# Performance work log

Hardware: AMD Instinct MI355X
Metric: run time of the kernel (lower is better)

The kernel has to match this reference:

```python
import jax, jax.numpy as jnp
import numpy as np

K = 3          # number of nearest neighbors (init kwarg k)
EPS = 1e-16    # PyG knn_interpolate clamps squared distance at 1e-16


def setup_inputs() -> dict:
    key = jax.random.key(0)
    ks = jax.random.split(key, 8)
    N, M, C_IN, C_SKIP, H = 4096, 16384, 256, 128, 256
    x = jax.random.normal(ks[0], (N, C_IN), dtype=jnp.float32)
    pos = jax.random.normal(ks[1], (N, 3), dtype=jnp.float32)
    x_skip = jax.random.normal(ks[2], (M, C_SKIP), dtype=jnp.float32)
    pos_skip = jax.random.normal(ks[3], (M, 3), dtype=jnp.float32)
    W1 = jax.random.normal(ks[4], (C_IN + C_SKIP, H), dtype=jnp.float32) * (1.0 / np.sqrt(C_IN + C_SKIP))
    b1 = jnp.zeros((H,), dtype=jnp.float32)
    W2 = jax.random.normal(ks[5], (H, H), dtype=jnp.float32) * (1.0 / np.sqrt(H))
    b2 = jnp.zeros((H,), dtype=jnp.float32)
    return {"x": x, "pos": pos, "x_skip": x_skip, "pos_skip": pos_skip,
            "W1": W1, "b1": b1, "W2": W2, "b2": b2}


def knn_interpolate(x, pos, pos_skip):
    # squared pairwise distances [M, N]
    d2 = (jnp.sum(pos_skip * pos_skip, -1, keepdims=True)
          - 2.0 * pos_skip @ pos.T
          + jnp.sum(pos * pos, -1))
    neg_d, idx = jax.lax.top_k(-d2, K)          # k smallest distances
    w = 1.0 / jnp.maximum(-neg_d, EPS)           # [M, K] inverse-distance weights
    feats = x[idx]                               # [M, K, C] gather
    return jnp.einsum('mk,mkc->mc', w, feats) / jnp.sum(w, -1, keepdims=True)


def reference(x, pos, x_skip, pos_skip, W1, b1, W2, b2):
    y = knn_interpolate(x, pos, pos_skip)                # [M, C_in]
    h = jnp.concatenate([y, x_skip], axis=-1)            # [M, C_in + C_skip]
    h = jax.nn.relu(h @ W1 + b1)
    return h @ W2 + b2                                    # [M, H]
```

## Files before the change

kernel.cpp:

```cpp
#include <hip/hip_runtime.h>
#include <hip/hip_bf16.h>

#define N_PTS 4096
#define M_PTS 16384
#define CIN   256
#define CSK   128
#define KDIM  384
#define HDIM  256
#define NSHARD 32
#define SHPTS (N_PTS / NSHARD)

typedef unsigned int  u32;
typedef unsigned short u16;
typedef __attribute__((ext_vector_type(8))) short bf16x8;
typedef __attribute__((ext_vector_type(4))) float f32x4;

__device__ __forceinline__ u16 f2bf(float f) {
    union { float f; u32 i; } w; w.f = f;
    u32 x = w.i;
    u32 r = x + 0x7fffu + ((x >> 16) & 1u);
    return (u16)(r >> 16);
}

__device__ __forceinline__ bool ltk(float s, int p, float t, int i) {
    return (s < t) || (s == t && p < i);
}
__device__ __forceinline__ void ins3(float s, int p,
                                     float& t0, float& t1, float& t2,
                                     int& i0, int& i1, int& i2) {
    if (ltk(s, p, t2, i2)) {
        if (ltk(s, p, t1, i1)) {
            t2 = t1; i2 = i1;
            if (ltk(s, p, t0, i0)) { t1 = t0; i1 = i0; t0 = s; i0 = p; }
            else                   { t1 = s;  i1 = p; }
        } else { t2 = s; i2 = p; }
    }
}

#define INS3BL(s, p, t0, t1, t2, i0, i1, i2)                              \
    {                                                                     \
        float _o0 = t0, _o1 = t1, _o2 = t2;                               \
        int _a0 = i0, _a1 = i1, _a2 = i2;                                 \
        bool _c0 = (s) < _o0, _c1 = (s) < _o1, _c2 = (s) < _o2;           \
        t0 = _c0 ? (s) : _o0;              i0 = _c0 ? (p) : _a0;          \
        t1 = _c0 ? _o0 : (_c1 ? (s) : _o1); i1 = _c0 ? _a0 : (_c1 ? (p) : _a1); \
        t2 = _c1 ? _o1 : (_c2 ? (s) : _o2); i2 = _c1 ? _a1 : (_c2 ? (p) : _a2); \
    }

#define INS3MM(s, p, t0, t1, t2, i0, i1, i2)                              \
    {                                                                     \
        bool _c0 = (s) < t0, _c1 = (s) < t1, _c2 = (s) < t2;              \
        int _oi0 = i0, _oi1 = i1;                                         \
        i0 = _c0 ? (p) : i0;                                              \
        i1 = _c0 ? _oi0 : (_c1 ? (p) : i1);                               \
        i2 = _c1 ? _oi1 : (_c2 ? (p) : i2);                               \
        float _ot0 = t0, _ot1 = t1;                                       \
        t0 = fminf(t0, (s));                                              \
        t1 = __builtin_amdgcn_fmed3f(_ot0, t1, (s));                      \
        t2 = __builtin_amdgcn_fmed3f(_ot1, t2, (s));                      \
    }

__global__ __launch_bounds__(256) void scanM_gemmZ_prep(
    const float* __restrict__ pos,
    const float* __restrict__ pos_skip,
    float* __restrict__ candM,
    const float* __restrict__ x,
    const float* __restrict__ W1,
    const float* __restrict__ W2,
    float* __restrict__ Z,
    u16* __restrict__ W1bT,
    u16* __restrict__ W2T)
{
    const int bid = blockIdx.x;
    const int tid = threadIdx.x;

    if (bid < 512) {
        __shared__ float4 spts[SHPTS];
        const int bx = bid & 15, sh = bid >> 4;
        const int pbase = sh * SHPTS;

        if (tid < SHPTS) {
            const int i = pbase + tid;
            float px = pos[3 * i], py = pos[3 * i + 1], pz = pos[3 * i + 2];
            float pn = __fadd_rn(__fadd_rn(__fmul_rn(px, px), __fmul_rn(py, py)),
                                 __fmul_rn(pz, pz));
            spts[tid] = make_float4(px, py, pz, pn);
        }

        const int mb = bx * 1024 + tid;
        float qx[4], qy[4], qz[4], qn[4];
        #pragma unroll
        for (int q = 0; q < 4; ++q) {
            const int m = mb + q * 256;
            qx[q] = pos_skip[3 * m];
            qy[q] = pos_skip[3 * m + 1];
            qz[q] = pos_skip[3 * m + 2];
            qn[q] = __fadd_rn(__fadd_rn(__fmul_rn(qx[q], qx[q]), __fmul_rn(qy[q], qy[q])),
                              __fmul_rn(qz[q], qz[q]));
        }
        __syncthreads();

        float e[4] = {3.4e38f, 3.4e38f, 3.4e38f, 3.4e38f};

        #pragma unroll 8
        for (int j = 0; j < SHPTS; ++j) {
            float4 v = spts[j];
            #pragma unroll
            for (int q = 0; q < 4; ++q) {
                float b = __fmaf_rn(qz[q], v.z, __fmaf_rn(qy[q], v.y, __fmul_rn(qx[q], v.x)));
                float s = __fadd_rn(__fmaf_rn(-2.0f, b, qn[q]), v.w);
                e[q] = fminf(e[q], s);
            }
        }

        #pragma unroll
        for (int q = 0; q < 4; ++q)
            candM[(size_t)sh * M_PTS + mb + q * 256] = e[q];
    } else if (bid < 640) {
        __shared__ alignas(16) u16 Bs[64][40];
        const int id = bid - 512;
        const int w = tid >> 6, l = tid & 63;
        const int bm = (id & 31) * 128;
        const int bn = (id >> 5) * 64;
        const int lr = l & 15, lg = l >> 4;

        f32x4 acc[2][4];
        #pragma unroll
        for (int mt = 0; mt < 2; ++mt)
            #pragma unroll
            for (int nt = 0; nt < 4; ++nt)
                acc[mt][nt] = (f32x4){0.f, 0.f, 0.f, 0.f};

        const int sc = tid >> 2;
        const int sk = (tid & 3) * 8;

        for (int k0 = 0; k0 < CIN; k0 += 32) {
            #pragma unroll
            for (int j = 0; j < 8; ++j)
                Bs[sc][sk + j] = f2bf(W1[(size_t)(k0 + sk + j) * HDIM + bn + sc]);
            __syncthreads();

            bf16x8 af[2];
            #pragma unroll
            for (int mt = 0; mt < 2; ++mt) {
                const float* xp = x + (size_t)(bm + w * 32 + mt * 16 + lr) * CIN + k0 + lg * 8;
                float4 h0 = *reinterpret_cast<const float4*>(xp);
                float4 h1 = *reinterpret_cast<const float4*>(xp + 4);
                af[mt][0] = (short)f2bf(h0.x); af[mt][1] = (short)f2bf(h0.y);
                af[mt][2] = (short)f2bf(h0.z); af[mt][3] = (short)f2bf(h0.w);
                af[mt][4] = (short)f2bf(h1.x); af[mt][5] = (short)f2bf(h1.y);
                af[mt][6] = (short)f2bf(h1.z); af[mt][7] = (short)f2bf(h1.w);
            }
            #pragma unroll
            for (int nt = 0; nt < 4; ++nt) {
                bf16x8 bf = *reinterpret_cast<const bf16x8*>(&Bs[nt * 16 + lr][lg * 8]);
                #pragma unroll
                for (int mt = 0; mt < 2; ++mt)
                    acc[mt][nt] = __builtin_amdgcn_mfma_f32_16x16x32_bf16(
                        af[mt], bf, acc[mt][nt], 0, 0, 0);
            }
            __syncthreads();
        }

        #pragma unroll
        for (int nt = 0; nt < 4; ++nt) {
            const int col = bn + nt * 16 + lr;
            #pragma unroll
            for (int mt = 0; mt < 2; ++mt)
                #pragma unroll
                for (int i = 0; i < 4; ++i) {
                    const int row = bm + w * 32 + mt * 16 + lg * 4 + i;
                    Z[(size_t)row * HDIM + col] = acc[mt][nt][i];
                }
        }
    } else {
        const int n = bid - 640;
        W2T[(size_t)n * HDIM + tid] = f2bf(W2[(size_t)tid * HDIM + n]);
        if (tid >= 128) {
            const int k = tid - 128;
            W1bT[(size_t)n * CSK + k] = f2bf(W1[(size_t)(CIN + k) * HDIM + n]);
        }
    }
}

__global__ __launch_bounds__(256) void knn_select_rescan(
    const float* __restrict__ pos,
    const float* __restrict__ pos_skip,
    const float* __restrict__ candM,
    float4* __restrict__ nbrw, uint4* __restrict__ nbri)
{
    __shared__ float sv[64][4][3];
    __shared__ int   si[64][4][3];
    __shared__ u32   ssel[64];
    const int tid  = threadIdx.x;
    const int ql   = tid >> 2;
    const int slot = tid & 3;
    const int m = blockIdx.x * 64 + ql;

    {
        float t0 = 3.4e38f, t1 = 3.4e38f, t2 = 3.4e38f;
        int   s0 = 63, s1 = 63, s2 = 63;
        #pragma unroll
        for (int k = 0; k < 8; ++k) {
            const int sh = slot * 8 + k;
            float mn = candM[(size_t)sh * M_PTS + m];
            INS3BL(mn, sh, t0, t1, t2, s0, s1, s2);
        }
        sv[ql][slot][0] = t0; sv[ql][slot][1] = t1; sv[ql][slot][2] = t2;
        si[ql][slot][0] = s0; si[ql][slot][1] = s1; si[ql][slot][2] = s2;
    }
    __syncthreads();
    if (slot == 0) {
        float t0 = 3.4e38f, t1 = 3.4e38f, t2 = 3.4e38f;
        int   s0 = 63, s1 = 63, s2 = 63;
        #pragma unroll
        for (int s = 0; s < 4; ++s)
            #pragma unroll
            for (int k = 0; k < 3; ++k)
                ins3(sv[ql][s][k], si[ql][s][k], t0, t1, t2, s0, s1, s2);
        ssel[ql] = (u32)s0 | ((u32)s1 << 8) | ((u32)s2 << 16);
    }
    __syncthreads();
    const u32 sel = ssel[ql];

    if (slot < 3) {
        const int sh = (sel >> (8 * slot)) & 63;
        const int pb = sh * SHPTS;

        const float qx = pos_skip[3 * m];
        const float qy = pos_skip[3 * m + 1];
        const float qz = pos_skip[3 * m + 2];
        const float qn = __fadd_rn(__fadd_rn(__fmul_rn(qx, qx), __fmul_rn(qy, qy)),
                                   __fmul_rn(qz, qz));

        float t0 = 3.4e38f, t1 = 3.4e38f, t2 = 3.4e38f;
        int   i0 = 0x7fffffff, i1 = 0x7fffffff, i2 = 0x7fffffff;

        #pragma unroll 4
        for (int j = 0; j < SHPTS; ++j) {
            const int p = pb + j;
            float px = pos[3 * p], py = pos[3 * p + 1], pz = pos[3 * p + 2];
            float pn = __fadd_rn(__fadd_rn(__fmul_rn(px, px), __fmul_rn(py, py)),
                                 __fmul_rn(pz, pz));
            float b = __fmaf_rn(qz, pz, __fmaf_rn(qy, py, __fmul_rn(qx, px)));
            float s = __fadd_rn(__fmaf_rn(-2.0f, b, qn), pn);
            INS3MM(s, p, t0, t1, t2, i0, i1, i2);
        }
        sv[ql][slot][0] = t0; sv[ql][slot][1] = t1; sv[ql][slot][2] = t2;
        si[ql][slot][0] = i0; si[ql][slot][1] = i1; si[ql][slot][2] = i2;
    }
    __syncthreads();

    if (slot == 0) {
        float t0 = 3.4e38f, t1 = 3.4e38f, t2 = 3.4e38f;
        int   i0 = 0x7fffffff, i1 = 0x7fffffff, i2 = 0x7fffffff;
        #pragma unroll
        for (int s = 0; s < 3; ++s)
            #pragma unroll
            for (int k = 0; k < 3; ++k)
                ins3(sv[ql][s][k], si[ql][s][k], t0, t1, t2, i0, i1, i2);

        float w0 = __fdiv_rn(1.0f, fmaxf(t0, 1e-16f));
        float w1 = __fdiv_rn(1.0f, fmaxf(t1, 1e-16f));
        float w2 = __fdiv_rn(1.0f, fmaxf(t2, 1e-16f));
        float inv = __fdiv_rn(1.0f, __fadd_rn(__fadd_rn(w0, w1), w2));
        nbrw[m] = make_float4(w0 * inv, w1 * inv, w2 * inv, 0.f);
        nbri[m] = make_uint4((u32)i0, (u32)i1, (u32)i2, 0u);
    }
}

__global__ __launch_bounds__(256) void gemm_SH(
    const float* __restrict__ x_skip, const u16* __restrict__ W1bT,
    const float* __restrict__ b1, const float* __restrict__ Z,
    const float4* __restrict__ nbrw, const uint4* __restrict__ nbri,
    u16* __restrict__ H)
{
    __shared__ alignas(16) u16 Bs[64][40];
    const int tid = threadIdx.x;
    const int w = tid >> 6, l = tid & 63;
    const int bm = blockIdx.x * 128;
    const int bn = blockIdx.y * 64;
    const int lr = l & 15, lg = l >> 4;

    f32x4 acc[2][4];
    #pragma unroll
    for (int mt = 0; mt < 2; ++mt)
        #pragma unroll
        for (int nt = 0; nt < 4; ++nt)
            acc[mt][nt] = (f32x4){0.f, 0.f, 0.f, 0.f};

    const int sc = tid >> 2;
    const int sk = (tid & 3) * 8;

    for (int k0 = 0; k0 < CSK; k0 += 32) {
        *reinterpret_cast<bf16x8*>(&Bs[sc][sk]) =
            *reinterpret_cast<const bf16x8*>(&W1bT[(size_t)(bn + sc) * CSK + k0 + sk]);
        __syncthreads();

        bf16x8 af[2];
        #pragma unroll
        for (int mt = 0; mt < 2; ++mt) {
            const float* xp = x_skip + (size_t)(bm + w * 32 + mt * 16 + lr) * CSK + k0 + lg * 8;
            float4 h0 = *reinterpret_cast<const float4*>(xp);
            float4 h1 = *reinterpret_cast<const float4*>(xp + 4);
            af[mt][0] = (short)f2bf(h0.x); af[mt][1] = (short)f2bf(h0.y);
            af[mt][2] = (short)f2bf(h0.z); af[mt][3] = (short)f2bf(h0.w);
            af[mt][4] = (short)f2bf(h1.x); af[mt][5] = (short)f2bf(h1.y);
            af[mt][6] = (short)f2bf(h1.z); af[mt][7] = (short)f2bf(h1.w);
        }
        #pragma unroll
        for (int nt = 0; nt < 4; ++nt) {
            bf16x8 bf = *reinterpret_cast<const bf16x8*>(&Bs[nt * 16 + lr][lg * 8]);
            #pragma unroll
            for (int mt = 0; mt < 2; ++mt)
                acc[mt][nt] = __builtin_amdgcn_mfma_f32_16x16x32_bf16(
                    af[mt], bf, acc[mt][nt], 0, 0, 0);
        }
        __syncthreads();
    }

    #pragma unroll
    for (int mt = 0; mt < 2; ++mt) {
        #pragma unroll
        for (int i = 0; i < 4; ++i) {
            const int row = bm + w * 32 + mt * 16 + lg * 4 + i;
            const float4 wv = nbrw[row];
            const uint4  iv = nbri[row];
            const float* z0 = Z + (size_t)(iv.x & 4095u) * HDIM;
            const float* z1 = Z + (size_t)(iv.y & 4095u) * HDIM;
            const float* z2 = Z + (size_t)(iv.z & 4095u) * HDIM;
            #pragma unroll
            for (int nt = 0; nt < 4; ++nt) {
                const int col = bn + nt * 16 + lr;
                float zb = wv.x * z0[col] + wv.y * z1[col] + wv.z * z2[col];
                float v = acc[mt][nt][i] + zb + b1[col];
                H[(size_t)row * HDIM + col] = f2bf(v > 0.f ? v : 0.f);
            }
        }
    }
}

__global__ __launch_bounds__(256) void gemm2_mfma(
    const u16* __restrict__ H, const u16* __restrict__ W2T,
    const float* __restrict__ b2, float* __restrict__ out)
{
    __shared__ alignas(16) u16 Bs[64][40];
    const int tid = threadIdx.x;
    const int w = tid >> 6, l = tid & 63;
    const int bm = blockIdx.x * 128;
    const int bn = blockIdx.y * 64;
    const int lr = l & 15, lg = l >> 4;

    f32x4 acc[2][4];
    #pragma unroll
    for (int mt = 0; mt < 2; ++mt)
        #pragma unroll
        for (int nt = 0; nt < 4; ++nt)
            acc[mt][nt] = (f32x4){0.f, 0.f, 0.f, 0.f};

    const int sc = tid >> 2;
    const int sk = (tid & 3) * 8;

    for (int k0 = 0; k0 < HDIM; k0 += 32) {
        *reinterpret_cast<bf16x8*>(&Bs[sc][sk]) =
            *reinterpret_cast<const bf16x8*>(&W2T[(size_t)(bn + sc) * HDIM + k0 + sk]);
        __syncthreads();

        bf16x8 af[2];
        #pragma unroll
        for (int mt = 0; mt < 2; ++mt) {
            const int row = bm + w * 32 + mt * 16 + lr;
            af[mt] = *reinterpret_cast<const bf16x8*>(H + (size_t)row * HDIM + k0 + lg * 8);
        }
        #pragma unroll
        for (int nt = 0; nt < 4; ++nt) {
            bf16x8 bf = *reinterpret_cast<const bf16x8*>(&Bs[nt * 16 + lr][lg * 8]);
            #pragma unroll
            for (int mt = 0; mt < 2; ++mt)
                acc[mt][nt] = __builtin_amdgcn_mfma_f32_16x16x32_bf16(
                    af[mt], bf, acc[mt][nt], 0, 0, 0);
        }
        __syncthreads();
    }

    #pragma unroll
    for (int nt = 0; nt < 4; ++nt) {
        const int col = bn + nt * 16 + lr;
        const float bias = b2[col];
        #pragma unroll
        for (int mt = 0; mt < 2; ++mt)
            #pragma unroll
            for (int i = 0; i < 4; ++i) {
                const int row = bm + w * 32 + mt * 16 + lg * 4 + i;
                out[(size_t)row * HDIM + col] = acc[mt][nt][i] + bias;
            }
    }
}

extern "C" void kernel_launch(void* const* d_in, const int* in_sizes, int n_in,
                              void* d_out, int out_size, void* d_ws, size_t ws_size,
                              hipStream_t stream) {
    const float* x        = (const float*)d_in[0];
    const float* pos      = (const float*)d_in[1];
    const float* x_skip   = (const float*)d_in[2];
    const float* pos_skip = (const float*)d_in[3];
    const float* W1       = (const float*)d_in[4];
    const float* b1       = (const float*)d_in[5];
    const float* W2       = (const float*)d_in[6];
    const float* b2       = (const float*)d_in[7];

    u16*    Hbuf = (u16*)d_ws;
    float*  Z    = (float*)((char*)d_ws + (8u << 20));
    float4* nbrw = (float4*)((char*)d_ws + (12u << 20));
    uint4*  nbri = (uint4*)((char*)d_ws + (12u << 20) + (256u << 10));
    u16*    W2T  = (u16*)((char*)d_ws + (12u << 20) + (512u << 10));
    u16*    W1bT = (u16*)((char*)d_ws + (12u << 20) + (640u << 10));

    float* candM = (float*)d_out;
    float* out   = (float*)d_out;

    scanM_gemmZ_prep <<<896, 256, 0, stream>>>(pos, pos_skip, candM, x, W1, W2,
                                               Z, W1bT, W2T);
    knn_select_rescan<<<256, 256, 0, stream>>>(pos, pos_skip, candM, nbrw, nbri);
    gemm_SH          <<<dim3(128, 4), 256, 0, stream>>>(x_skip, W1bT, b1, Z, nbrw, nbri, Hbuf);
    gemm2_mfma       <<<dim3(128, 4), 256, 0, stream>>>(Hbuf, W2T, b2, out);
}
```

Before: 60.65 us.

## Fuse kNN selection into first GEMM and double queries per scan thread

The kNN select/rescan kernel is merged into the skip-GEMM kernel. Neighbor weights and indices now pass through shared memory instead of global buffers, which removes one launch and a global round-trip. Because the grid is (256,2), each 64-row block's selection and rescan now runs twice, once per column half. The shard-scan phase also handles 8 queries per thread over 256 blocks instead of 4 over 512, which adds register pressure and lowers parallelism in exchange for more reuse of each loaded point.

Result: slower. 66.37 us (+9.4%).

```diff
diff --git a/kernel.cpp b/kernel.cpp
--- a/kernel.cpp
+++ b/kernel.cpp
@@ -74,9 +74,9 @@
     const int bid = blockIdx.x;
     const int tid = threadIdx.x;
 
-    if (bid < 512) {
+    if (bid < 256) {
         __shared__ float4 spts[SHPTS];
-        const int bx = bid & 15, sh = bid >> 4;
+        const int bx = bid & 7, sh = bid >> 3;
         const int pbase = sh * SHPTS;
 
         if (tid < SHPTS) {
@@ -87,10 +87,10 @@
             spts[tid] = make_float4(px, py, pz, pn);
         }
 
-        const int mb = bx * 1024 + tid;
-        float qx[4], qy[4], qz[4], qn[4];
-        #pragma unroll
-        for (int q = 0; q < 4; ++q) {
+        const int mb = bx * 2048 + tid;
+        float qx[8], qy[8], qz[8], qn[8];
+        #pragma unroll
+        for (int q = 0; q < 8; ++q) {
             const int m = mb + q * 256;
             qx[q] = pos_skip[3 * m];
             qy[q] = pos_skip[3 * m + 1];
@@ -100,13 +100,14 @@
         }
         __syncthreads();
 
-        float e[4] = {3.4e38f, 3.4e38f, 3.4e38f, 3.4e38f};
-
-        #pragma unroll 8
+        float e[8] = {3.4e38f, 3.4e38f, 3.4e38f, 3.4e38f,
+                      3.4e38f, 3.4e38f, 3.4e38f, 3.4e38f};
+
+        #pragma unroll 4
         for (int j = 0; j < SHPTS; ++j) {
             float4 v = spts[j];
             #pragma unroll
-            for (int q = 0; q < 4; ++q) {
+            for (int q = 0; q < 8; ++q) {
                 float b = __fmaf_rn(qz[q], v.z, __fmaf_rn(qy[q], v.y, __fmul_rn(qx[q], v.x)));
                 float s = __fadd_rn(__fmaf_rn(-2.0f, b, qn[q]), v.w);
                 e[q] = fminf(e[q], s);
@@ -114,11 +115,11 @@
         }
 
         #pragma unroll
-        for (int q = 0; q < 4; ++q)
+        for (int q = 0; q < 8; ++q)
             candM[(size_t)sh * M_PTS + mb + q * 256] = e[q];
-    } else if (bid < 640) {
+    } else if (bid < 384) {
         __shared__ alignas(16) u16 Bs[64][40];
-        const int id = bid - 512;
+        const int id = bid - 256;
         const int w = tid >> 6, l = tid & 63;
         const int bm = (id & 31) * 128;
         const int bn = (id >> 5) * 64;
@@ -174,7 +175,7 @@
                 }
         }
     } else {
-        const int n = bid - 640;
+        const int n = bid - 384;
         W2T[(size_t)n * HDIM + tid] = f2bf(W2[(size_t)tid * HDIM + n]);
         if (tid >= 128) {
             const int k = tid - 128;
@@ -183,19 +184,27 @@
     }
 }
 
-__global__ __launch_bounds__(256) void knn_select_rescan(
+__global__ __launch_bounds__(256) void gemm_SHsel(
     const float* __restrict__ pos,
     const float* __restrict__ pos_skip,
     const float* __restrict__ candM,
-    float4* __restrict__ nbrw, uint4* __restrict__ nbri)
+    const float* __restrict__ x_skip, const u16* __restrict__ W1bT,
+    const float* __restrict__ b1, const float* __restrict__ Z,
+    u16* __restrict__ H)
 {
     __shared__ float sv[64][4][3];
     __shared__ int   si[64][4][3];
     __shared__ u32   ssel[64];
+    __shared__ float4 nw[64];
+    __shared__ uint4  ni[64];
+    __shared__ alignas(16) u16 Bs[128][40];
+
     const int tid  = threadIdx.x;
     const int ql   = tid >> 2;
     const int slot = tid & 3;
-    const int m = blockIdx.x * 64 + ql;
+    const int bm   = blockIdx.x * 64;
+    const int bn   = blockIdx.y * 128;
+    const int m    = bm + ql;
 
     {
         float t0 = 3.4e38f, t1 = 3.4e38f, t2 = 3.4e38f;
@@ -264,78 +273,60 @@
         float w1 = __fdiv_rn(1.0f, fmaxf(t1, 1e-16f));
         float w2 = __fdiv_rn(1.0f, fmaxf(t2, 1e-16f));
         float inv = __fdiv_rn(1.0f, __fadd_rn(__fadd_rn(w0, w1), w2));
-        nbrw[m] = make_float4(w0 * inv, w1 * inv, w2 * inv, 0.f);
-        nbri[m] = make_uint4((u32)i0, (u32)i1, (u32)i2, 0u);
-    }
-}
-
-__global__ __launch_bounds__(256) void gemm_SH(
-    const float* __restrict__ x_skip, const u16* __restrict__ W1bT,
-    const float* __restrict__ b1, const float* __restrict__ Z,
-    const float4* __restrict__ nbrw, const uint4* __restrict__ nbri,
-    u16* __restrict__ H)
-{
-    __shared__ alignas(16) u16 Bs[64][40];
-    const int tid = threadIdx.x;
+        nw[ql] = make_float4(w0 * inv, w1 * inv, w2 * inv, 0.f);
+        ni[ql] = make_uint4((u32)i0, (u32)i1, (u32)i2, 0u);
+    }
+    __syncthreads();
+
     const int w = tid >> 6, l = tid & 63;
-    const int bm = blockIdx.x * 128;
-    const int bn = blockIdx.y * 64;
     const int lr = l & 15, lg = l >> 4;
 
-    f32x4 acc[2][4];
+    f32x4 acc[8];
     #pragma unroll
-    for (int mt = 0; mt < 2; ++mt)
-        #pragma unroll
-        for (int nt = 0; nt < 4; ++nt)
-            acc[mt][nt] = (f32x4){0.f, 0.f, 0.f, 0.f};
-
-    const int sc = tid >> 2;
-    const int sk = (tid & 3) * 8;
+    for (int nt = 0; nt < 8; ++nt) acc[nt] = (f32x4){0.f, 0.f, 0.f, 0.f};
+
+    const int sc = tid >> 1;
+    const int sk = (tid & 1) * 16;
 
     for (int k0 = 0; k0 < CSK; k0 += 32) {
         *reinterpret_cast<bf16x8*>(&Bs[sc][sk]) =
             *reinterpret_cast<const bf16x8*>(&W1bT[(size_t)(bn + sc) * CSK + k0 + sk]);
+        *reinterpret_cast<bf16x8*>(&Bs[sc][sk + 8]) =
+            *reinterpret_cast<const bf16x8*>(&W1bT[(size_t)(bn + sc) * CSK + k0 + sk + 8]);
         __syncthreads();
 
-        bf16x8 af[2];
-        #pragma unroll
-        for (int mt = 0; mt < 2; ++mt) {
-            const float* xp = x_skip + (size_t)(bm + w * 32 + mt * 16 + lr) * CSK + k0 + lg * 8;
-            float4 h0 = *reinterpret_cast<const float4*>(xp);
-            float4 h1 = *reinterpret_cast<const float4*>(xp + 4);
-            af[mt][0] = (short)f2bf(h0.x); af[mt][1] = (short)f2bf(h0.y);
-            af[mt][2] = (short)f2bf(h0.z); af[mt][3] = (short)f2bf(h0.w);
-            af[mt][4] = (short)f2bf(h1.x); af[mt][5] = (short)f2bf(h1.y);
-            af[mt][6] = (short)f2bf(h1.z); af[mt][7] = (short)f2bf(h1.w);
-        }
-        #pragma unroll
-        for (int nt = 0; nt < 4; ++nt) {
+        const float* xp = x_skip + (size_t)(bm + w * 16 + lr) * CSK + k0 + lg * 8;
+        float4 h0 = *reinterpret_cast<const float4*>(xp);
+        float4 h1 = *reinterpret_cast<const float4*>(xp + 4);
+        bf16x8 af;
+        af[0] = (short)f2bf(h0.x); af[1] = (short)f2bf(h0.y);
+        af[2] = (short)f2bf(h0.z); af[3] = (short)f2bf(h0.w);
+        af[4] = (short)f2bf(h1.x); af[5] = (short)f2bf(h1.y);
+        af[6] = (short)f2bf(h1.z); af[7] = (short)f2bf(h1.w);
+
+        #pragma unroll
+        for (int nt = 0; nt < 8; ++nt) {
             bf16x8 bf = *reinterpret_cast<const bf16x8*>(&Bs[nt * 16 + lr][lg * 8]);
-            #pragma unroll
-            for (int mt = 0; mt < 2; ++mt)
-                acc[mt][nt] = __builtin_amdgcn_mfma_f32_16x16x32_bf16(
-                    af[mt], bf, acc[mt][nt], 0, 0, 0);
+            acc[nt] = __builtin_amdgcn_mfma_f32_16x16x32_bf16(af, bf, acc[nt], 0, 0, 0);
         }
         __syncthreads();
     }
 
     #pragma unroll
-    for (int mt = 0; mt < 2; ++mt) {
-        #pragma unroll
-        for (int i = 0; i < 4; ++i) {
-            const int row = bm + w * 32 + mt * 16 + lg * 4 + i;
-            const float4 wv = nbrw[row];
-            const uint4  iv = nbri[row];
-            const float* z0 = Z + (size_t)(iv.x & 4095u) * HDIM;
-            const float* z1 = Z + (size_t)(iv.y & 4095u) * HDIM;
-            const float* z2 = Z + (size_t)(iv.z & 4095u) * HDIM;
-            #pragma unroll
-            for (int nt = 0; nt < 4; ++nt) {
-                const int col = bn + nt * 16 + lr;
-                float zb = wv.x * z0[col] + wv.y * z1[col] + wv.z * z2[col];
-                float v = acc[mt][nt][i] + zb + b1[col];
-                H[(size_t)row * HDIM + col] = f2bf(v > 0.f ? v : 0.f);
-            }
+    for (int i = 0; i < 4; ++i) {
+        const int lrow = w * 16 + lg * 4 + i;
+        const int row  = bm + lrow;
+        const float4 wv = nw[lrow];
+        const uint4  iv = ni[lrow];
+        const float* z0 = Z + (size_t)(iv.x & 4095u) * HDIM;
+        const float* z1 = Z + (size_t)(iv.y & 4095u) * HDIM;
+        const float* z2 = Z + (size_t)(iv.z & 4095u) * HDIM;
+        #pragma unroll
+        for (int nt = 0; nt < 8; ++nt) {
+            const int col = bn + nt * 16 + lr;
+            float zb = wv.x * z0[col] + wv.y * z1[col] + wv.z * z2[col];
+            float v = acc[nt][i] + zb + b1[col];
+            H[(size_t)row * HDIM + col] = f2bf(v > 0.f ? v : 0.f);
         }
     }
 }
@@ -411,17 +402,15 @@
 
     u16*    Hbuf = (u16*)d_ws;
     float*  Z    = (float*)((char*)d_ws + (8u << 20));
-    float4* nbrw = (float4*)((char*)d_ws + (12u << 20));
-    uint4*  nbri = (uint4*)((char*)d_ws + (12u << 20) + (256u << 10));
-    u16*    W2T  = (u16*)((char*)d_ws + (12u << 20) + (512u << 10));
-    u16*    W1bT = (u16*)((char*)d_ws + (12u << 20) + (640u << 10));
+    u16*    W2T  = (u16*)((char*)d_ws + (12u << 20));
+    u16*    W1bT = (u16*)((char*)d_ws + (12u << 20) + (128u << 10));
 
     float* candM = (float*)d_out;
     float* out   = (float*)d_out;
 
-    scanM_gemmZ_prep <<<896, 256, 0, stream>>>(pos, pos_skip, candM, x, W1, W2,
+    scanM_gemmZ_prep <<<640, 256, 0, stream>>>(pos, pos_skip, candM, x, W1, W2,
                                                Z, W1bT, W2T);
-    knn_select_rescan<<<256, 256, 0, stream>>>(pos, pos_skip, candM, nbrw, nbri);
-    gemm_SH          <<<dim3(128, 4), 256, 0, stream>>>(x_skip, W1bT, b1, Z, nbrw, nbri, Hbuf);
+    gemm_SHsel       <<<dim3(256, 2), 256, 0, stream>>>(pos, pos_skip, candM,
+                                                        x_skip, W1bT, b1, Z, Hbuf);
     gemm2_mfma       <<<dim3(128, 4), 256, 0, stream>>>(Hbuf, W2T, b2, out);
 }
```
